# Optimization experiments

Measured on AMD Instinct MI355X. Metric: run time of the kernel, lower is better.

Reference implementation:

```python
import jax, jax.numpy as jnp
import numpy as np

BATCH, T, N_STATE, N_CTRL = 16, 512, 64, 32


def setup_inputs() -> dict:
    key = jax.random.key(0)
    ks = jax.random.split(key, 6)
    n, m = N_STATE, N_CTRL
    # SPD per-step cost: Q = M M^T/(n+m) + I  (guarantees Q_uu invertible)
    M = jax.random.normal(ks[0], (BATCH, T, n + m, n + m), jnp.float32)
    Q = jnp.einsum('btij,btkj->btik', M, M) / (n + m) + jnp.eye(n + m, dtype=jnp.float32)
    p = jax.random.normal(ks[1], (BATCH, T, n + m), jnp.float32)
    # near-stable dynamics so the T-step rollout stays bounded
    A = 0.9 * jnp.eye(n, dtype=jnp.float32) + 0.02 * jax.random.normal(ks[2], (BATCH, T, n, n), jnp.float32)
    B = 0.1 * jax.random.normal(ks[3], (BATCH, T, n, m), jnp.float32)
    c1 = 0.1 * jax.random.normal(ks[4], (BATCH, T, n), jnp.float32)
    x_init = jax.random.normal(ks[5], (BATCH, n), jnp.float32)
    return {'Q': Q, 'p': p, 'A': A, 'B': B, 'c1': c1, 'x_init': x_init}


def _lqr(Q, p, A, B, c1, x_init):
    n = A.shape[-1]
    F = jnp.concatenate([A, B], axis=-1)                      # [b,T,n,n+m]
    # time-major for scan
    Qs = jnp.moveaxis(Q, 1, 0)
    ps = jnp.moveaxis(p, 1, 0)
    Fs = jnp.moveaxis(F, 1, 0)
    cs = jnp.moveaxis(c1, 1, 0)
    bsz = x_init.shape[0]
    V0 = jnp.zeros((bsz, n, n), Q.dtype)
    v0 = jnp.zeros((bsz, n), Q.dtype)

    def bstep(carry, inp):
        V, v = carry
        Qt, pt, Ft, ct = inp
        FtV = jnp.einsum('bij,bik->bjk', Ft, V)               # F^T V : [b,n+m,n]
        Qh = Qt + FtV @ Ft                                     # Q_t + F^T V F
        qh = pt + jnp.einsum('bij,bi->bj', Ft,
                             jnp.einsum('bij,bj->bi', V, ct) + v)
        Quu, Qux = Qh[:, n:, n:], Qh[:, n:, :n]
        Qxx, Qxu = Qh[:, :n, :n], Qh[:, :n, n:]
        qx, qu = qh[:, :n], qh[:, n:]
        L = jnp.linalg.cholesky(Quu)
        rhs = jnp.concatenate([Qux, qu[..., None]], axis=-1)   # solve K and k together
        sol = -jax.scipy.linalg.cho_solve((L, True), rhs)
        K, k = sol[..., :n], sol[..., n]
        QuuK = Quu @ K
        Vn = Qxx + Qxu @ K + jnp.einsum('bji,bjk->bik', K, Qux + QuuK)
        Vn = 0.5 * (Vn + jnp.swapaxes(Vn, -1, -2))             # keep symmetric
        vn = qx + jnp.einsum('bij,bj->bi', Qxu, k) \
             + jnp.einsum('bji,bj->bi', K, qu + jnp.einsum('bij,bj->bi', Quu, k))
        return (Vn, vn), (K, k)

    _, (Ks, ks) = jax.lax.scan(bstep, (V0, v0), (Qs, ps, Fs, cs), reverse=True)

    def fstep(x, inp):
        Kt, kt, At, Bt, ct = inp
        u = jnp.einsum('bij,bj->bi', Kt, x) + kt
        xn = jnp.einsum('bij,bj->bi', At, x) + jnp.einsum('bij,bj->bi', Bt, u) + ct
        return xn, (x, u)

    _, (xs, us) = jax.lax.scan(fstep, x_init,
                               (Ks, ks, jnp.moveaxis(A, 1, 0), jnp.moveaxis(B, 1, 0), cs))
    tau = jnp.concatenate([xs, us], axis=-1)                   # [T,b,n+m]
    return jnp.moveaxis(tau, 0, 1)                             # [b,T,n+m]


def reference(Q, p, A, B, c1, x_init):
    return _lqr(Q, p, A, B, c1, x_init)
```

## Files before the change

### kernel.cpp

```cpp
#include <hip/hip_runtime.h>
#include <math.h>

#define TT 512
#define NB 16

#define QH_B   0
#define LI_B   38400
#define T1_B   43008
#define VBH_B  52368
#define VBL_B  61584
#define FTH_B  70800
#define FTL_B  84624
#define WTH_B  98448
#define WTL_B  112272
#define T1PH_B 126096
#define T1PL_B 131216
#define T1MH_B 136336
#define T1ML_B 141456
#define QHF_B  146576
#define VV_B   146960
#define CV_B   147216
#define SMB    147600

#define AB0 0
#define AB1 6400
#define KF0 12800
#define KF1 14976
#define XB0 17152
#define XB1 17216
#define UBO 17280
#define AXO 17312

#define WSK_STRIDE 2080

typedef __attribute__((ext_vector_type(8))) short s8v;
typedef __attribute__((ext_vector_type(4))) float f4v;

__device__ __forceinline__ float lanebc(float x, int lane) {
    return __int_as_float(__builtin_amdgcn_readlane(__float_as_int(x), lane));
}
__device__ __forceinline__ float dot4(float4 a, float4 b) {
    return a.x * b.x + a.y * b.y + a.z * b.z + a.w * b.w;
}
__device__ __forceinline__ unsigned short f2bf(float x) {
    unsigned int u = __float_as_uint(x);
    u += 0x7FFFu + ((u >> 16) & 1u);
    return (unsigned short)(u >> 16);
}
__device__ __forceinline__ float bf2f(unsigned short h) {
    return __uint_as_float(((unsigned int)h) << 16);
}
__device__ __forceinline__ void pack4(const f4v d, ushort4* hp, ushort4* lp) {
    unsigned short h0 = f2bf(d[0]), h1 = f2bf(d[1]), h2 = f2bf(d[2]), h3 = f2bf(d[3]);
    *hp = make_ushort4(h0, h1, h2, h3);
    *lp = make_ushort4(f2bf(d[0] - bf2f(h0)), f2bf(d[1] - bf2f(h1)),
                       f2bf(d[2] - bf2f(h2)), f2bf(d[3] - bf2f(h3)));
}
__device__ __forceinline__ void tileMN(int T, int& mt, int& nt) {
    mt = (T >= 15) ? 5 : (T >= 10) ? 4 : (T >= 6) ? 3 : (T >= 3) ? 2 : (T >= 1) ? 1 : 0;
    nt = T - mt * (mt + 1) / 2;
}
#define MFMA(a,b,c) __builtin_amdgcn_mfma_f32_16x16x32_bf16((a),(b),(c),0,0,0)

__launch_bounds__(512, 2)
__global__ void lqr_kernel(const float* __restrict__ Q, const float* __restrict__ P,
                           const float* __restrict__ A, const float* __restrict__ B,
                           const float* __restrict__ c1, const float* __restrict__ xinit,
                           float* __restrict__ out, float* __restrict__ ws)
{
    __shared__ __align__(16) unsigned char smb[SMB];
    float*          QHf = (float*)(smb + QH_B);
    float*          LIf = (float*)(smb + LI_B);
    float*          T1f = (float*)(smb + T1_B);
    unsigned short* VBH = (unsigned short*)(smb + VBH_B);
    unsigned short* VBL = (unsigned short*)(smb + VBL_B);
    unsigned short* FTH = (unsigned short*)(smb + FTH_B);
    unsigned short* FTL = (unsigned short*)(smb + FTL_B);
    unsigned short* WTH = (unsigned short*)(smb + WTH_B);
    unsigned short* WTL = (unsigned short*)(smb + WTL_B);
    unsigned short* T1PH = (unsigned short*)(smb + T1PH_B);
    unsigned short* T1PL = (unsigned short*)(smb + T1PL_B);
    unsigned short* T1MH = (unsigned short*)(smb + T1MH_B);
    unsigned short* T1ML = (unsigned short*)(smb + T1ML_B);
    float*          QHF = (float*)(smb + QHF_B);
    float*          VVf = (float*)(smb + VV_B);
    float*          CVf = (float*)(smb + CV_B);

    const int tid = threadIdx.x;
    const int b   = blockIdx.x;
    const int wv  = tid >> 6;
    const int ln  = tid & 63;
    const int l15 = ln & 15;
    const int lq  = ln >> 4;
    float* wsK = ws;

    const int qcnt = (wv < 5) ? 3 : 2;
    const int qr = ln >> 2, qc4 = ln & 3;

    float4 qreg[3];
    {
        const float* Qg = Q + ((size_t)b * TT + (TT - 1)) * 9216;
#pragma unroll
        for (int tt = 0; tt < 3; ++tt) if (tt < qcnt) {
            int T = wv + 8 * tt, mt, nt; tileMN(T, mt, nt);
            qreg[tt] = *(const float4*)&Qg[(16 * mt + qr) * 96 + 16 * nt + 4 * qc4];
        }
    }

    if (tid < 384) {
        const size_t bt = (size_t)b * TT + (TT - 1);
        const int rb = tid & 15, cb = tid >> 4;
        float4 fr[4];
#pragma unroll
        for (int r = 0; r < 4; ++r) {
            const float* src = (cb < 16) ? (A + (bt * 64 + 4 * rb + r) * 64 + 4 * cb)
                                         : (B + (bt * 64 + 4 * rb + r) * 32 + 4 * (cb - 16));
            fr[r] = *(const float4*)src;
        }
#pragma unroll
        for (int c2 = 0; c2 < 4; ++c2) {
            f4v col;
            col[0] = ((const float*)&fr[0])[c2]; col[1] = ((const float*)&fr[1])[c2];
            col[2] = ((const float*)&fr[2])[c2]; col[3] = ((const float*)&fr[3])[c2];
            ushort4 hv, lv; pack4(col, &hv, &lv);
            *(ushort4*)&FTH[(4 * cb + c2) * 72 + 4 * rb] = hv;
            *(ushort4*)&FTL[(4 * cb + c2) * 72 + 4 * rb] = lv;
        }
    } else {
        float* vb = (float*)VBH;
        for (int i = tid - 384; i < 4608; i += 128) vb[i] = 0.0f;
        if (tid >= 448) VVf[tid - 448] = 0.0f;
    }
    __syncthreads();

    for (int t = TT - 1; t >= 0; --t) {
        const size_t bt  = (size_t)b * TT + t;
        const size_t btp = (size_t)b * TT + ((t > 0) ? (t - 1) : 0);

#pragma unroll
        for (int tt = 0; tt < 3; ++tt) if (tt < qcnt) {
            int T = wv + 8 * tt, mt, nt; tileMN(T, mt, nt);
            *(float4*)&QHf[(16 * mt + qr) * 100 + 16 * nt + 4 * qc4] = qreg[tt];
        }
        {
            const float* Qg = Q + btp * 9216;
#pragma unroll
            for (int tt = 0; tt < 3; ++tt) if (tt < qcnt) {
                int T = wv + 8 * tt, mt, nt; tileMN(T, mt, nt);
                qreg[tt] = *(const float4*)&Qg[(16 * mt + qr) * 96 + 16 * nt + 4 * qc4];
            }
        }
        float4 fp4[4];
        if (wv >= 1 && wv <= 6) {
            const int tau = tid - 64, rb = tau & 15, cb = tau >> 4;
#pragma unroll
            for (int r = 0; r < 4; ++r) {
                const float* src = (cb < 16) ? (A + (btp * 64 + 4 * rb + r) * 64 + 4 * cb)
                                             : (B + (btp * 64 + 4 * rb + r) * 32 + 4 * (cb - 16));
                fp4[r] = *(const float4*)src;
            }
        }
        if (wv == 7 && ln < 16)
            *(float4*)&CVf[4 * ln] = *(const float4*)&c1[bt * 64 + 4 * ln];
        float pv = 0.0f;
        if (ln < 48 && (ln & 3) == 0) pv = P[bt * 96 + 12 * wv + (ln >> 2)];

        auto g1Tile = [&](int mt, int nt) {
            const unsigned short* ah = VBH + (16 * nt + l15) * 72 + 8 * lq;
            const unsigned short* al = VBL + (16 * nt + l15) * 72 + 8 * lq;
            const unsigned short* bh = FTH + (16 * mt + l15) * 72 + 8 * lq;
            const unsigned short* bl = FTL + (16 * mt + l15) * 72 + 8 * lq;
            f4v d = {0.0f, 0.0f, 0.0f, 0.0f};
#pragma unroll
            for (int kc = 0; kc < 2; ++kc) {
                s8v Ah = *(const s8v*)(ah + 32 * kc);
                s8v Al = *(const s8v*)(al + 32 * kc);
                s8v Bh = *(const s8v*)(bh + 32 * kc);
                s8v Bl = *(const s8v*)(bl + 32 * kc);
                d = MFMA(Ah, Bh, d);
                d = MFMA(Ah, Bl, d);
                d = MFMA(Al, Bh, d);
            }
            int wi = 16 * nt + 4 * lq, wc = 16 * mt + l15;
            ushort4 hv, lv; pack4(d, &hv, &lv);
            *(ushort4*)&WTH[wc * 72 + wi] = hv;
            *(ushort4*)&WTL[wc * 72 + wi] = lv;
        };
        auto qhTile = [&](int T) {
            int mt, nt; tileMN(T, mt, nt);
            int orow = 16 * mt + 4 * lq, ocol = 16 * nt + l15;
            const unsigned short* ah = FTH + (16 * mt + l15) * 72 + 8 * lq;
            const unsigned short* al = FTL + (16 * mt + l15) * 72 + 8 * lq;
            const unsigned short* bh = WTH + (16 * nt + l15) * 72 + 8 * lq;
            const unsigned short* bl = WTL + (16 * nt + l15) * 72 + 8 * lq;
            f4v d;
#pragma unroll
            for (int rr = 0; rr < 4; ++rr)
                d[rr] = QHf[(orow + rr) * 100 + ocol];
#pragma unroll
            for (int kc = 0; kc < 2; ++kc) {
                s8v Ah = *(const s8v*)(ah + 32 * kc);
                s8v Al = *(const s8v*)(al + 32 * kc);
                s8v Bh = *(const s8v*)(bh + 32 * kc);
                s8v Bl = *(const s8v*)(bl + 32 * kc);
                d = MFMA(Ah, Bh, d);
                d = MFMA(Ah, Bl, d);
                d = MFMA(Al, Bh, d);
            }
#pragma unroll
            for (int rr = 0; rr < 4; ++rr)
                QHf[(orow + rr) * 100 + ocol] = d[rr];
            if (mt > nt) {
#pragma unroll
                for (int rr = 0; rr < 4; ++rr)
                    QHf[ocol * 100 + orow + rr] = d[rr];
            }
        };

        {
            g1Tile(4 + (wv >> 2), wv & 3);
            if (ln < 48) {
                int row = 12 * wv + (ln >> 2), kq = ln & 3;
                float acc = 0.0f;
                const unsigned short* fh = FTH + row * 72 + 16 * kq;
                const unsigned short* fl = FTL + row * 72 + 16 * kq;
                const float* vvp = VVf + 16 * kq;
#pragma unroll
                for (int k = 0; k < 16; ++k)
                    acc += (bf2f(fh[k]) + bf2f(fl[k])) * vvp[k];
                acc += __shfl_xor(acc, 1);
                acc += __shfl_xor(acc, 2);
                if ((ln & 3) == 0) QHF[row] = acc + pv;
            }
        }
        __syncthreads();

        if (wv == 0) {
            qhTile(14); qhTile(19); qhTile(20);
        } else {
            int g0 = wv - 1;  g1Tile(g0 >> 2, g0 & 3);
            int g1 = 6 + wv;  g1Tile(g1 >> 2, g1 & 3);
            if (wv <= 2) { int g2 = 13 + wv; g1Tile(g2 >> 2, g2 & 3); }
        }
        __syncthreads();

        if (wv == 0) {
            __builtin_amdgcn_s_setprio(1);
            const int i = ln & 31;
            float a[32];
#pragma unroll
            for (int j4 = 0; j4 < 8; ++j4) {
                float4 v = *(const float4*)&QHf[(64 + i) * 100 + 64 + 4 * j4];
                a[4 * j4] = v.x; a[4 * j4 + 1] = v.y; a[4 * j4 + 2] = v.z; a[4 * j4 + 3] = v.w;
            }
#pragma unroll
            for (int j = 0; j < 32; ++j) {
                float dj = lanebc(a[j], j);
                float rj = rsqrtf(dj);
                a[j] *= rj;
#pragma unroll
                for (int k = j + 1; k < 32; ++k)
                    a[k] -= a[j] * lanebc(a[j], k);
            }
            float y[32];
#pragma unroll
            for (int r = 0; r < 32; ++r) {
                float acc0 = (r == i) ? 1.0f : 0.0f, acc1 = 0.0f;
#pragma unroll
                for (int j = 0; j < r; ++j) {
                    float lrj = lanebc(a[j], r);
                    if (j & 1) acc1 -= lrj * y[j]; else acc0 -= lrj * y[j];
                }
                y[r] = (acc0 + acc1) * __builtin_amdgcn_rcpf(lanebc(a[r], r));
            }
            __builtin_amdgcn_s_setprio(0);
            if (ln < 32) {
#pragma unroll
                for (int r = 0; r < 32; ++r) LIf[r * 36 + ln] = y[r];
            }
        } else if (wv == 7) {
#pragma unroll
            for (int pass = 0; pass < 2; ++pass) {
                int j = pass ? (64 + (ln & 31)) : ln;
                if (pass && ln >= 32) break;
                float acc = QHF[j];
                const unsigned short* wh = WTH + j * 72;
                const unsigned short* wl = WTL + j * 72;
#pragma unroll 4
                for (int i = 0; i < 64; ++i)
                    acc += (bf2f(wh[i]) + bf2f(wl[i])) * CVf[i];
                QHf[j * 100 + 96] = acc;
            }
        } else {
            int ta, tb, tc;
            switch (wv) {
                case 1: ta = 10; tb = 15; tc = 0; break;
                case 2: ta = 11; tb = 16; tc = 1; break;
                case 3: ta = 12; tb = 17; tc = 2; break;
                case 4: ta = 13; tb = 18; tc = 3; break;
                case 5: ta = 4;  tb = 5;  tc = 6; break;
                default: ta = 7; tb = 8;  tc = 9; break;
            }
            qhTile(ta); qhTile(tb); qhTile(tc);
        }
        __syncthreads();

        {
            const int c = tid & 63, rq = tid >> 6;
            f4v acc = {0.0f, 0.0f, 0.0f, 0.0f};
#pragma unroll
            for (int j4 = 0; j4 < 8; ++j4) {
                float4 qv = *(const float4*)&QHf[c * 100 + 64 + 4 * j4];
#pragma unroll
                for (int rr = 0; rr < 4; ++rr) {
                    float4 li = *(const float4*)&LIf[(4 * rq + rr) * 36 + 4 * j4];
                    acc[rr] += dot4(li, qv);
                }
            }
            *(f4v*)&T1f[c * 36 + 4 * rq] = acc;
            {
                ushort4 ph, pl; pack4(acc, &ph, &pl);
                *(ushort4*)&T1PH[c * 40 + 4 * rq] = ph;
                *(ushort4*)&T1PL[c * 40 + 4 * rq] = pl;
                ushort4 mh = make_ushort4((unsigned short)(ph.x ^ 0x8000u), (unsigned short)(ph.y ^ 0x8000u),
                                          (unsigned short)(ph.z ^ 0x8000u), (unsigned short)(ph.w ^ 0x8000u));
                ushort4 ml = make_ushort4((unsigned short)(pl.x ^ 0x8000u), (unsigned short)(pl.y ^ 0x8000u),
                                          (unsigned short)(pl.z ^ 0x8000u), (unsigned short)(pl.w ^ 0x8000u));
                *(ushort4*)&T1MH[c * 40 + 4 * rq] = mh;
                *(ushort4*)&T1ML[c * 40 + 4 * rq] = ml;
            }
            if (tid < 32) {
                float aq = 0.0f;
#pragma unroll 4
                for (int j = 0; j < 32; ++j)
                    aq += LIf[tid * 36 + j] * QHf[(64 + j) * 100 + 96];
                T1f[64 * 36 + tid] = aq;
            }
            if (wv >= 1 && wv <= 6) {
                const int tau = tid - 64, rb = tau & 15, cb = tau >> 4;
#pragma unroll
                for (int c2 = 0; c2 < 4; ++c2) {
                    f4v col;
                    col[0] = ((const float*)&fp4[0])[c2]; col[1] = ((const float*)&fp4[1])[c2];
                    col[2] = ((const float*)&fp4[2])[c2]; col[3] = ((const float*)&fp4[3])[c2];
                    ushort4 hv, lv; pack4(col, &hv, &lv);
                    *(ushort4*)&FTH[(4 * cb + c2) * 72 + 4 * rb] = hv;
                    *(ushort4*)&FTL[(4 * cb + c2) * 72 + 4 * rb] = lv;
                }
            }
        }
        __syncthreads();

        {
            const int c = tid & 63, jq = tid >> 6;
            f4v acc = {0.0f, 0.0f, 0.0f, 0.0f};
#pragma unroll
            for (int i4 = 0; i4 < 8; ++i4) {
                float4 tv = *(const float4*)&T1f[c * 36 + 4 * i4];
#pragma unroll
                for (int ii = 0; ii < 4; ++ii) {
                    float4 li = *(const float4*)&LIf[(4 * i4 + ii) * 36 + 4 * jq];
                    float tvi = (ii == 0) ? tv.x : (ii == 1) ? tv.y : (ii == 2) ? tv.z : tv.w;
                    acc[0] += tvi * li.x; acc[1] += tvi * li.y;
                    acc[2] += tvi * li.z; acc[3] += tvi * li.w;
                }
            }
            float* wrow = wsK + bt * WSK_STRIDE;
#pragma unroll
            for (int jj = 0; jj < 4; ++jj)
                wrow[(4 * jq + jj) * 65 + c] = -acc[jj];
            if (tid < 32) {
                float aq = 0.0f;
#pragma unroll 4
                for (int i = 0; i < 32; ++i)
                    aq += LIf[i * 36 + tid] * T1f[64 * 36 + i];
                wsK[bt * WSK_STRIDE + tid * 65 + 64] = -aq;
            }
#pragma unroll
            for (int tt = 0; tt < 2; ++tt) {
                int T = 2 * wv + tt, mt = T >> 2, nt = T & 3;
                f4v d;
#pragma unroll
                for (int rr = 0; rr < 4; ++rr)
                    d[rr] = QHf[(16 * nt + 4 * lq + rr) * 100 + 16 * mt + l15];
                s8v Ah = *(const s8v*)(T1MH + (16 * nt + l15) * 40 + 8 * lq);
                s8v Al = *(const s8v*)(T1ML + (16 * nt + l15) * 40 + 8 * lq);
                s8v Bh = *(const s8v*)(T1PH + (16 * mt + l15) * 40 + 8 * lq);
                s8v Bl = *(const s8v*)(T1PL + (16 * mt + l15) * 40 + 8 * lq);
                d = MFMA(Ah, Bh, d);
                d = MFMA(Ah, Bl, d);
                d = MFMA(Al, Bh, d);
                ushort4 hv, lv; pack4(d, &hv, &lv);
                *(ushort4*)&VBH[(16 * mt + l15) * 72 + 16 * nt + 4 * lq] = hv;
                *(ushort4*)&VBL[(16 * mt + l15) * 72 + 16 * nt + 4 * lq] = lv;
            }
            {
                int r = 8 * wv + (ln >> 3), kq = ln & 7;
                float4 t1r = *(const float4*)&T1f[r * 36 + 4 * kq];
                float4 t1q = *(const float4*)&T1f[64 * 36 + 4 * kq];
                float acc2 = dot4(t1r, t1q);
                acc2 += __shfl_xor(acc2, 1);
                acc2 += __shfl_xor(acc2, 2);
                acc2 += __shfl_xor(acc2, 4);
                if (kq == 0) VVf[r] = QHf[r * 100 + 96] - acc2;
            }
        }
        __syncthreads();
    }

    float* sm = (float*)smb;
    {
        const size_t bt0 = (size_t)b * TT;
#pragma unroll
        for (int it = 0; it < 3; ++it) {
            int q = tid + 512 * it, row = q / 24, g = q % 24;
            const float* src = (g < 16) ? (A + (bt0 * 64 + row) * 64 + 4 * g)
                                        : (B + (bt0 * 64 + row) * 32 + 4 * (g - 16));
            *(float4*)&sm[AB0 + row * 100 + 4 * g] = *(const float4*)src;
        }
#pragma unroll
        for (int i = 0; i < 5; ++i) {
            int idx = tid + 512 * i;
            if (idx < 2080) {
                int j = idx / 65, c = idx - 65 * j;
                sm[KF0 + j * 68 + c] = wsK[bt0 * WSK_STRIDE + idx];
            }
        }
        if (tid < 64) sm[XB0 + tid] = xinit[b * 64 + tid];
    }
    __syncthreads();

    for (int t = 0; t < TT; ++t) {
        const size_t bt  = (size_t)b * TT + t;
        const size_t btn = (size_t)b * TT + ((t < TT - 1) ? (t + 1) : t);
        const int cur = t & 1;
        const int abC = cur ? AB1 : AB0, abN = cur ? AB0 : AB1;
        const int kfC = cur ? KF1 : KF0, kfN = cur ? KF0 : KF1;
        const int xbC = cur ? XB1 : XB0, xbN = cur ? XB0 : XB1;

        float4 abpre[6];
        float kpre[9];
        float cpre = 0.0f;
        if (tid >= 256) {
            const int t2 = tid - 256;
#pragma unroll
            for (int it = 0; it < 6; ++it) {
                int q = t2 + 256 * it, row = q / 24, g = q % 24;
                const float* src = (g < 16) ? (A + (btn * 64 + row) * 64 + 4 * g)
                                            : (B + (btn * 64 + row) * 32 + 4 * (g - 16));
                abpre[it] = *(const float4*)src;
            }
#pragma unroll
            for (int i = 0; i < 9; ++i) {
                int idx = t2 + 256 * i;
                kpre[i] = (idx < 2080) ? wsK[btn * WSK_STRIDE + idx] : 0.0f;
            }
            cpre = c1[bt * 64 + ((tid - 256) >> 2)];
        }

        if (tid < 256) {
            const int j = tid >> 3, q = tid & 7;
            float4 k0 = *(const float4*)&sm[kfC + j * 68 + 8 * q];
            float4 k1 = *(const float4*)&sm[kfC + j * 68 + 8 * q + 4];
            float4 x0 = *(const float4*)&sm[xbC + 8 * q];
            float4 x1 = *(const float4*)&sm[xbC + 8 * q + 4];
            float pa = dot4(k0, x0) + dot4(k1, x1);
            pa += __shfl_xor(pa, 1);
            pa += __shfl_xor(pa, 2);
            pa += __shfl_xor(pa, 4);
            if (q == 0) {
                float u = pa + sm[kfC + j * 68 + 64];
                sm[UBO + j] = u;
                out[bt * 96 + 64 + j] = u;
            }
        } else {
            const int r = (tid - 256) >> 2, q = tid & 3;
            float pa = 0.0f;
#pragma unroll
            for (int e4 = 0; e4 < 4; ++e4) {
                float4 av = *(const float4*)&sm[abC + r * 100 + 16 * q + 4 * e4];
                float4 xv = *(const float4*)&sm[xbC + 16 * q + 4 * e4];
                pa += dot4(av, xv);
            }
            pa += __shfl_xor(pa, 1);
            pa += __shfl_xor(pa, 2);
            if (q == 0) sm[AXO + r] = pa + cpre;
            if (q == 1) out[bt * 96 + r] = sm[xbC + r];
        }
        __syncthreads();

        if (tid < 256) {
            const int r = tid >> 2, q = tid & 3;
            float4 b0 = *(const float4*)&sm[abC + r * 100 + 64 + 8 * q];
            float4 b1 = *(const float4*)&sm[abC + r * 100 + 64 + 8 * q + 4];
            float4 u0 = *(const float4*)&sm[UBO + 8 * q];
            float4 u1 = *(const float4*)&sm[UBO + 8 * q + 4];
            float pa = dot4(b0, u0) + dot4(b1, u1);
            pa += __shfl_xor(pa, 1);
            pa += __shfl_xor(pa, 2);
            if (q == 0) sm[xbN + r] = sm[AXO + r] + pa;
        } else {
            const int t2 = tid - 256;
#pragma unroll
            for (int it = 0; it < 6; ++it) {
                int q = t2 + 256 * it, row = q / 24, g = q % 24;
                *(float4*)&sm[abN + row * 100 + 4 * g] = abpre[it];
            }
#pragma unroll
            for (int i = 0; i < 9; ++i) {
                int idx = t2 + 256 * i;
                if (idx < 2080) {
                    int j = idx / 65, c = idx - 65 * j;
                    sm[kfN + j * 68 + c] = kpre[i];
                }
            }
        }
        __syncthreads();
    }
}

extern "C" void kernel_launch(void* const* d_in, const int* in_sizes, int n_in,
                              void* d_out, int out_size, void* d_ws, size_t ws_size,
                              hipStream_t stream) {
    (void)in_sizes; (void)n_in; (void)out_size;
    const float* Q  = (const float*)d_in[0];
    const float* p  = (const float*)d_in[1];
    const float* A  = (const float*)d_in[2];
    const float* B  = (const float*)d_in[3];
    const float* c1 = (const float*)d_in[4];
    const float* xi = (const float*)d_in[5];
    if (ws_size < (size_t)NB * TT * WSK_STRIDE * sizeof(float)) return;
    lqr_kernel<<<NB, 512, 0, stream>>>(Q, p, A, B, c1, xi, (float*)d_out, (float*)d_ws);
}
```

Baseline: 8.355 ms.

## Widen block to 768 threads and rebalance per-step work across twelve waves

Raises the block from 8 to 12 wavefronts and redistributes the backward-pass tile work: G1 and QH tiles, the q-hat vector, the F staging loads and the V update tiles are reassigned so each wave does less serial work per time step. One barrier stage is merged by overlapping the Cholesky wave with qhTile work, and dedicated waves now handle prefetch of F and the p/c1 loads. The forward rollout uses the extra waves for prefetch. More waves per block may raise register pressure under the new launch bounds, and block-wide barriers now cost more to synchronize, while only 16 blocks run.

```diff
diff --git a/kernel.cpp b/kernel.cpp
--- a/kernel.cpp
+++ b/kernel.cpp
@@ -62,7 +62,7 @@
 }
 #define MFMA(a,b,c) __builtin_amdgcn_mfma_f32_16x16x32_bf16((a),(b),(c),0,0,0)
 
-__launch_bounds__(512, 2)
+__launch_bounds__(768, 3)
 __global__ void lqr_kernel(const float* __restrict__ Q, const float* __restrict__ P,
                            const float* __restrict__ A, const float* __restrict__ B,
                            const float* __restrict__ c1, const float* __restrict__ xinit,
@@ -94,17 +94,30 @@
     const int lq  = ln >> 4;
     float* wsK = ws;
 
-    const int qcnt = (wv < 5) ? 3 : 2;
+    int qT0, qT1;
+    switch (wv) {
+        case 0:  qT0 = 14; qT1 = 19; break;
+        case 1:  qT0 = 20; qT1 = 0;  break;
+        case 2:  qT0 = 1;  qT1 = 2;  break;
+        case 3:  qT0 = 3;  qT1 = 4;  break;
+        case 4:  qT0 = 5;  qT1 = 6;  break;
+        case 5:  qT0 = 7;  qT1 = 8;  break;
+        case 6:  qT0 = 9;  qT1 = 10; break;
+        case 7:  qT0 = 11; qT1 = 12; break;
+        case 8:  qT0 = 13; qT1 = 15; break;
+        case 9:  qT0 = 16; qT1 = 17; break;
+        case 10: qT0 = 18; qT1 = -1; break;
+        default: qT0 = -1; qT1 = -1; break;
+    }
     const int qr = ln >> 2, qc4 = ln & 3;
 
-    float4 qreg[3];
+    float4 qreg[2];
     {
         const float* Qg = Q + ((size_t)b * TT + (TT - 1)) * 9216;
-#pragma unroll
-        for (int tt = 0; tt < 3; ++tt) if (tt < qcnt) {
-            int T = wv + 8 * tt, mt, nt; tileMN(T, mt, nt);
-            qreg[tt] = *(const float4*)&Qg[(16 * mt + qr) * 96 + 16 * nt + 4 * qc4];
-        }
+        if (qT0 >= 0) { int mt, nt; tileMN(qT0, mt, nt);
+            qreg[0] = *(const float4*)&Qg[(16 * mt + qr) * 96 + 16 * nt + 4 * qc4]; }
+        if (qT1 >= 0) { int mt, nt; tileMN(qT1, mt, nt);
+            qreg[1] = *(const float4*)&Qg[(16 * mt + qr) * 96 + 16 * nt + 4 * qc4]; }
     }
 
     if (tid < 384) {
@@ -128,8 +141,8 @@
         }
     } else {
         float* vb = (float*)VBH;
-        for (int i = tid - 384; i < 4608; i += 128) vb[i] = 0.0f;
-        if (tid >= 448) VVf[tid - 448] = 0.0f;
+        for (int i = tid - 384; i < 4608; i += 384) vb[i] = 0.0f;
+        if (tid >= 384 && tid < 448) VVf[tid - 384] = 0.0f;
     }
     __syncthreads();
 
@@ -137,33 +150,39 @@
         const size_t bt  = (size_t)b * TT + t;
         const size_t btp = (size_t)b * TT + ((t > 0) ? (t - 1) : 0);
 
-#pragma unroll
-        for (int tt = 0; tt < 3; ++tt) if (tt < qcnt) {
-            int T = wv + 8 * tt, mt, nt; tileMN(T, mt, nt);
-            *(float4*)&QHf[(16 * mt + qr) * 100 + 16 * nt + 4 * qc4] = qreg[tt];
-        }
+        if (qT0 >= 0) { int mt, nt; tileMN(qT0, mt, nt);
+            *(float4*)&QHf[(16 * mt + qr) * 100 + 16 * nt + 4 * qc4] = qreg[0]; }
+        if (qT1 >= 0) { int mt, nt; tileMN(qT1, mt, nt);
+            *(float4*)&QHf[(16 * mt + qr) * 100 + 16 * nt + 4 * qc4] = qreg[1]; }
         {
             const float* Qg = Q + btp * 9216;
-#pragma unroll
-            for (int tt = 0; tt < 3; ++tt) if (tt < qcnt) {
-                int T = wv + 8 * tt, mt, nt; tileMN(T, mt, nt);
-                qreg[tt] = *(const float4*)&Qg[(16 * mt + qr) * 96 + 16 * nt + 4 * qc4];
-            }
-        }
-        float4 fp4[4];
-        if (wv >= 1 && wv <= 6) {
-            const int tau = tid - 64, rb = tau & 15, cb = tau >> 4;
-#pragma unroll
-            for (int r = 0; r < 4; ++r) {
-                const float* src = (cb < 16) ? (A + (btp * 64 + 4 * rb + r) * 64 + 4 * cb)
-                                             : (B + (btp * 64 + 4 * rb + r) * 32 + 4 * (cb - 16));
-                fp4[r] = *(const float4*)src;
-            }
-        }
-        if (wv == 7 && ln < 16)
-            *(float4*)&CVf[4 * ln] = *(const float4*)&c1[bt * 64 + 4 * ln];
-        float pv = 0.0f;
-        if (ln < 48 && (ln & 3) == 0) pv = P[bt * 96 + 12 * wv + (ln >> 2)];
+            if (qT0 >= 0) { int mt, nt; tileMN(qT0, mt, nt);
+                qreg[0] = *(const float4*)&Qg[(16 * mt + qr) * 96 + 16 * nt + 4 * qc4]; }
+            if (qT1 >= 0) { int mt, nt; tileMN(qT1, mt, nt);
+                qreg[1] = *(const float4*)&Qg[(16 * mt + qr) * 96 + 16 * nt + 4 * qc4]; }
+        }
+        float4 fpa[4], fpb[4];
+        if (tid >= 512) {
+            const int tau = tid - 512;
+            {
+                const int rb = tau & 15, cb = tau >> 4;
+#pragma unroll
+                for (int r = 0; r < 4; ++r) {
+                    const float* src = (cb < 16) ? (A + (btp * 64 + 4 * rb + r) * 64 + 4 * cb)
+                                                 : (B + (btp * 64 + 4 * rb + r) * 32 + 4 * (cb - 16));
+                    fpa[r] = *(const float4*)src;
+                }
+            }
+            if (tau < 128) {
+                const int be = tau + 256, rb = be & 15, cb = be >> 4;
+#pragma unroll
+                for (int r = 0; r < 4; ++r) {
+                    const float* src = (cb < 16) ? (A + (btp * 64 + 4 * rb + r) * 64 + 4 * cb)
+                                                 : (B + (btp * 64 + 4 * rb + r) * 32 + 4 * (cb - 16));
+                    fpb[r] = *(const float4*)src;
+                }
+            }
+        }
 
         auto g1Tile = [&](int mt, int nt) {
             const unsigned short* ah = VBH + (16 * nt + l15) * 72 + 8 * lq;
@@ -217,34 +236,36 @@
             }
         };
 
-        {
-            g1Tile(4 + (wv >> 2), wv & 3);
-            if (ln < 48) {
-                int row = 12 * wv + (ln >> 2), kq = ln & 3;
-                float acc = 0.0f;
-                const unsigned short* fh = FTH + row * 72 + 16 * kq;
-                const unsigned short* fl = FTL + row * 72 + 16 * kq;
-                const float* vvp = VVf + 16 * kq;
-#pragma unroll
-                for (int k = 0; k < 16; ++k)
-                    acc += (bf2f(fh[k]) + bf2f(fl[k])) * vvp[k];
-                acc += __shfl_xor(acc, 1);
-                acc += __shfl_xor(acc, 2);
-                if ((ln & 3) == 0) QHF[row] = acc + pv;
+        if (wv == 0) {
+            g1Tile(4, 0); g1Tile(4, 1); g1Tile(4, 2); g1Tile(4, 3);
+            qhTile(14);
+        } else if (wv == 1) {
+            g1Tile(5, 0); g1Tile(5, 1); g1Tile(5, 2); g1Tile(5, 3);
+            qhTile(20);
+        } else if (wv <= 9) {
+            int g = 2 * (wv - 2);
+            g1Tile(g >> 2, g & 3);
+            g1Tile((g + 1) >> 2, (g + 1) & 3);
+        } else {
+            const int lam = tid - 640;
+            float pvv = 0.0f;
+            if (lam < 96) pvv = P[bt * 96 + lam];
+            if (lam >= 96 && lam < 112)
+                *(float4*)&CVf[4 * (lam - 96)] = *(const float4*)&c1[bt * 64 + 4 * (lam - 96)];
+            if (lam < 96) {
+                float acc = pvv;
+                const unsigned short* fh = FTH + lam * 72;
+                const unsigned short* fl = FTL + lam * 72;
+#pragma unroll 4
+                for (int k = 0; k < 64; ++k)
+                    acc += (bf2f(fh[k]) + bf2f(fl[k])) * VVf[k];
+                QHF[lam] = acc;
             }
         }
         __syncthreads();
 
         if (wv == 0) {
-            qhTile(14); qhTile(19); qhTile(20);
-        } else {
-            int g0 = wv - 1;  g1Tile(g0 >> 2, g0 & 3);
-            int g1 = 6 + wv;  g1Tile(g1 >> 2, g1 & 3);
-            if (wv <= 2) { int g2 = 13 + wv; g1Tile(g2 >> 2, g2 & 3); }
-        }
-        __syncthreads();
-
-        if (wv == 0) {
+            qhTile(19);
             __builtin_amdgcn_s_setprio(1);
             const int i = ln & 31;
             float a[32];
@@ -278,11 +299,23 @@
 #pragma unroll
                 for (int r = 0; r < 32; ++r) LIf[r * 36 + ln] = y[r];
             }
-        } else if (wv == 7) {
-#pragma unroll
-            for (int pass = 0; pass < 2; ++pass) {
-                int j = pass ? (64 + (ln & 31)) : ln;
-                if (pass && ln >= 32) break;
+        } else if (wv <= 9) {
+            int ta, tb;
+            switch (wv) {
+                case 1: ta = 10; tb = 11; break;
+                case 2: ta = 12; tb = 13; break;
+                case 3: ta = 15; tb = 16; break;
+                case 4: ta = 17; tb = 18; break;
+                case 5: ta = 0;  tb = 1;  break;
+                case 6: ta = 2;  tb = 3;  break;
+                case 7: ta = 4;  tb = 5;  break;
+                case 8: ta = 6;  tb = 7;  break;
+                default: ta = 8; tb = 9;  break;
+            }
+            qhTile(ta); qhTile(tb);
+        } else {
+            int j = (wv == 10) ? ln : (64 + ln);
+            if (wv == 10 || ln < 32) {
                 float acc = QHF[j];
                 const unsigned short* wh = WTH + j * 72;
                 const unsigned short* wl = WTL + j * 72;
@@ -291,21 +324,10 @@
                     acc += (bf2f(wh[i]) + bf2f(wl[i])) * CVf[i];
                 QHf[j * 100 + 96] = acc;
             }
-        } else {
-            int ta, tb, tc;
-            switch (wv) {
-                case 1: ta = 10; tb = 15; tc = 0; break;
-                case 2: ta = 11; tb = 16; tc = 1; break;
-                case 3: ta = 12; tb = 17; tc = 2; break;
-                case 4: ta = 13; tb = 18; tc = 3; break;
-                case 5: ta = 4;  tb = 5;  tc = 6; break;
-                default: ta = 7; tb = 8;  tc = 9; break;
-            }
-            qhTile(ta); qhTile(tb); qhTile(tc);
         }
         __syncthreads();
 
-        {
+        if (tid < 512) {
             const int c = tid & 63, rq = tid >> 6;
             f4v acc = {0.0f, 0.0f, 0.0f, 0.0f};
 #pragma unroll
@@ -336,22 +358,53 @@
                     aq += LIf[tid * 36 + j] * QHf[(64 + j) * 100 + 96];
                 T1f[64 * 36 + tid] = aq;
             }
-            if (wv >= 1 && wv <= 6) {
-                const int tau = tid - 64, rb = tau & 15, cb = tau >> 4;
+        } else {
+            const int tau = tid - 512;
+            {
+                const int rb = tau & 15, cb = tau >> 4;
 #pragma unroll
                 for (int c2 = 0; c2 < 4; ++c2) {
                     f4v col;
-                    col[0] = ((const float*)&fp4[0])[c2]; col[1] = ((const float*)&fp4[1])[c2];
-                    col[2] = ((const float*)&fp4[2])[c2]; col[3] = ((const float*)&fp4[3])[c2];
+                    col[0] = ((const float*)&fpa[0])[c2]; col[1] = ((const float*)&fpa[1])[c2];
+                    col[2] = ((const float*)&fpa[2])[c2]; col[3] = ((const float*)&fpa[3])[c2];
                     ushort4 hv, lv; pack4(col, &hv, &lv);
                     *(ushort4*)&FTH[(4 * cb + c2) * 72 + 4 * rb] = hv;
                     *(ushort4*)&FTL[(4 * cb + c2) * 72 + 4 * rb] = lv;
                 }
             }
+            if (tau < 128) {
+                const int be = tau + 256, rb = be & 15, cb = be >> 4;
+#pragma unroll
+                for (int c2 = 0; c2 < 4; ++c2) {
+                    f4v col;
+                    col[0] = ((const float*)&fpb[0])[c2]; col[1] = ((const float*)&fpb[1])[c2];
+                    col[2] = ((const float*)&fpb[2])[c2]; col[3] = ((const float*)&fpb[3])[c2];
+                    ushort4 hv, lv; pack4(col, &hv, &lv);
+                    *(ushort4*)&FTH[(4 * cb + c2) * 72 + 4 * rb] = hv;
+                    *(ushort4*)&FTL[(4 * cb + c2) * 72 + 4 * rb] = lv;
+                }
+            }
         }
         __syncthreads();
 
-        {
+        auto vnTile = [&](int T) {
+            int mt = T >> 2, nt = T & 3;
+            f4v d;
+#pragma unroll
+            for (int rr = 0; rr < 4; ++rr)
+                d[rr] = QHf[(16 * nt + 4 * lq + rr) * 100 + 16 * mt + l15];
+            s8v Ah = *(const s8v*)(T1MH + (16 * nt + l15) * 40 + 8 * lq);
+            s8v Al = *(const s8v*)(T1ML + (16 * nt + l15) * 40 + 8 * lq);
+            s8v Bh = *(const s8v*)(T1PH + (16 * mt + l15) * 40 + 8 * lq);
+            s8v Bl = *(const s8v*)(T1PL + (16 * mt + l15) * 40 + 8 * lq);
+            d = MFMA(Ah, Bh, d);
+            d = MFMA(Ah, Bl, d);
+            d = MFMA(Al, Bh, d);
+            ushort4 hv, lv; pack4(d, &hv, &lv);
+            *(ushort4*)&VBH[(16 * mt + l15) * 72 + 16 * nt + 4 * lq] = hv;
+            *(ushort4*)&VBL[(16 * mt + l15) * 72 + 16 * nt + 4 * lq] = lv;
+        };
+        if (tid < 512) {
             const int c = tid & 63, jq = tid >> 6;
             f4v acc = {0.0f, 0.0f, 0.0f, 0.0f};
 #pragma unroll
@@ -376,32 +429,19 @@
                     aq += LIf[i * 36 + tid] * T1f[64 * 36 + i];
                 wsK[bt * WSK_STRIDE + tid * 65 + 64] = -aq;
             }
-#pragma unroll
-            for (int tt = 0; tt < 2; ++tt) {
-                int T = 2 * wv + tt, mt = T >> 2, nt = T & 3;
-                f4v d;
-#pragma unroll
-                for (int rr = 0; rr < 4; ++rr)
-                    d[rr] = QHf[(16 * nt + 4 * lq + rr) * 100 + 16 * mt + l15];
-                s8v Ah = *(const s8v*)(T1MH + (16 * nt + l15) * 40 + 8 * lq);
-                s8v Al = *(const s8v*)(T1ML + (16 * nt + l15) * 40 + 8 * lq);
-                s8v Bh = *(const s8v*)(T1PH + (16 * mt + l15) * 40 + 8 * lq);
-                s8v Bl = *(const s8v*)(T1PL + (16 * mt + l15) * 40 + 8 * lq);
-                d = MFMA(Ah, Bh, d);
-                d = MFMA(Ah, Bl, d);
-                d = MFMA(Al, Bh, d);
-                ushort4 hv, lv; pack4(d, &hv, &lv);
-                *(ushort4*)&VBH[(16 * mt + l15) * 72 + 16 * nt + 4 * lq] = hv;
-                *(ushort4*)&VBL[(16 * mt + l15) * 72 + 16 * nt + 4 * lq] = lv;
-            }
+            vnTile(wv);
+        } else {
+            vnTile(8 + 2 * (wv - 8));
+            vnTile(9 + 2 * (wv - 8));
             {
-                int r = 8 * wv + (ln >> 3), kq = ln & 7;
-                float4 t1r = *(const float4*)&T1f[r * 36 + 4 * kq];
-                float4 t1q = *(const float4*)&T1f[64 * 36 + 4 * kq];
-                float acc2 = dot4(t1r, t1q);
+                int r = 16 * (wv - 8) + (ln >> 2), kq = ln & 3;
+                float4 a1 = *(const float4*)&T1f[r * 36 + 8 * kq];
+                float4 a2 = *(const float4*)&T1f[r * 36 + 8 * kq + 4];
+                float4 b1 = *(const float4*)&T1f[64 * 36 + 8 * kq];
+                float4 b2 = *(const float4*)&T1f[64 * 36 + 8 * kq + 4];
+                float acc2 = dot4(a1, b1) + dot4(a2, b2);
                 acc2 += __shfl_xor(acc2, 1);
                 acc2 += __shfl_xor(acc2, 2);
-                acc2 += __shfl_xor(acc2, 4);
                 if (kq == 0) VVf[r] = QHf[r * 100 + 96] - acc2;
             }
         }
@@ -412,15 +452,18 @@
     {
         const size_t bt0 = (size_t)b * TT;
 #pragma unroll
-        for (int it = 0; it < 3; ++it) {
-            int q = tid + 512 * it, row = q / 24, g = q % 24;
-            const float* src = (g < 16) ? (A + (bt0 * 64 + row) * 64 + 4 * g)
-                                        : (B + (bt0 * 64 + row) * 32 + 4 * (g - 16));
-            *(float4*)&sm[AB0 + row * 100 + 4 * g] = *(const float4*)src;
-        }
-#pragma unroll
-        for (int i = 0; i < 5; ++i) {
-            int idx = tid + 512 * i;
+        for (int it = 0; it < 2; ++it) {
+            int q = tid + 768 * it;
+            if (q < 1536) {
+                int row = q / 24, g = q % 24;
+                const float* src = (g < 16) ? (A + (bt0 * 64 + row) * 64 + 4 * g)
+                                            : (B + (bt0 * 64 + row) * 32 + 4 * (g - 16));
+                *(float4*)&sm[AB0 + row * 100 + 4 * g] = *(const float4*)src;
+            }
+        }
+#pragma unroll
+        for (int i = 0; i < 3; ++i) {
+            int idx = tid + 768 * i;
             if (idx < 2080) {
                 int j = idx / 65, c = idx - 65 * j;
                 sm[KF0 + j * 68 + c] = wsK[bt0 * WSK_STRIDE + idx];
@@ -441,8 +484,8 @@
         float4 abpre[6];
         float kpre[9];
         float cpre = 0.0f;
-        if (tid >= 256) {
-            const int t2 = tid - 256;
+        if (tid >= 512) {
+            const int t2 = tid - 512;
 #pragma unroll
             for (int it = 0; it < 6; ++it) {
                 int q = t2 + 256 * it, row = q / 24, g = q % 24;
@@ -455,8 +498,9 @@
                 int idx = t2 + 256 * i;
                 kpre[i] = (idx < 2080) ? wsK[btn * WSK_STRIDE + idx] : 0.0f;
             }
+        }
+        if (tid >= 256 && tid < 512)
             cpre = c1[bt * 64 + ((tid - 256) >> 2)];
-        }
 
         if (tid < 256) {
             const int j = tid >> 3, q = tid & 7;
@@ -473,7 +517,7 @@
                 sm[UBO + j] = u;
                 out[bt * 96 + 64 + j] = u;
             }
-        } else {
+        } else if (tid < 512) {
             const int r = (tid - 256) >> 2, q = tid & 3;
             float pa = 0.0f;
 #pragma unroll
@@ -499,8 +543,8 @@
             pa += __shfl_xor(pa, 1);
             pa += __shfl_xor(pa, 2);
             if (q == 0) sm[xbN + r] = sm[AXO + r] + pa;
-        } else {
-            const int t2 = tid - 256;
+        } else if (tid >= 512) {
+            const int t2 = tid - 512;
 #pragma unroll
             for (int it = 0; it < 6; ++it) {
                 int q = t2 + 256 * it, row = q / 24, g = q % 24;
@@ -530,5 +574,5 @@
     const float* c1 = (const float*)d_in[4];
     const float* xi = (const float*)d_in[5];
     if (ws_size < (size_t)NB * TT * WSK_STRIDE * sizeof(float)) return;
-    lqr_kernel<<<NB, 512, 0, stream>>>(Q, p, A, B, c1, xi, (float*)d_out, (float*)d_ws);
-}
+    lqr_kernel<<<NB, 768, 0, stream>>>(Q, p, A, B, c1, xi, (float*)d_out, (float*)d_ws);
+}
```

Result: slower. 10.25 ms (+22.7%).
